# Kernel tuning notes

Hardware: AMD Instinct MI355X
Metric: run time of the kernel (lower is better)

## Reference

```python
import jax, jax.numpy as jnp
import numpy as np

EMBED = 768
HEADS = 12
HEAD_DIM = EMBED // HEADS
RATES = (1, 2, 4)
SEGS = (2048, 4096, 8192)


def setup_inputs() -> dict:
    key = jax.random.key(0)
    k1, k2, k3 = jax.random.split(key, 3)
    b, n = 2, 8192
    x = jax.random.normal(k1, (b, n, EMBED), dtype=jnp.float32)
    Wqkv = jax.random.normal(k2, (3 * EMBED, EMBED), dtype=jnp.float32) * 0.02
    Wout = jax.random.normal(k3, (EMBED, EMBED), dtype=jnp.float32) * 0.02
    return {"x": x, "Wqkv": Wqkv, "Wout": Wout}


def _dilated_attention(qkv):
    # qkv: [b, n, 3, h, d]
    b, n, _, h, d = qkv.shape
    scale = 1.0 / jnp.sqrt(jnp.asarray(d, qkv.dtype))
    out = jnp.zeros((b, n, h, d), dtype=qkv.dtype)
    for r, s in zip(RATES, SEGS):
        sr = s // r
        nseg = n // s
        # strided gather: [b, nseg, sr, 3, h, d]
        g = qkv.reshape(b, nseg, s, 3, h, d)[:, :, ::r]
        # fold stride offset into batch; attention runs over the segment axis
        g = g.transpose(0, 2, 1, 3, 4, 5).reshape(b * sr, nseg, 3, h, d)
        q, k, v = g[:, :, 0], g[:, :, 1], g[:, :, 2]
        scores = jnp.einsum('bnhd,bmhd->bhnm', q, k) * scale
        attn = jax.nn.softmax(scores, axis=-1)
        o = jnp.einsum('bhnm,bmhd->bnhd', attn, v)
        # scatter-add back into strided positions
        o = o.reshape(b, sr, nseg, h, d).transpose(0, 2, 1, 3, 4)
        out = out.reshape(b, nseg, s, h, d).at[:, :, ::r].add(o).reshape(b, n, h, d)
    # normalize over full sequence dim (as in original module)
    out = out / out.sum(axis=1, keepdims=True)
    return out


def reference(x, Wqkv, Wout):
    b, n, e = x.shape
    qkv = (x @ Wqkv.T).reshape(b, n, 3, HEADS, HEAD_DIM)
    o = _dilated_attention(qkv)  # [b, n, h, d]
    return o.reshape(b, n, e) @ Wout.T
```

## Files before the change

kernel.cpp:

```cpp
#include <hip/hip_runtime.h>

typedef unsigned short u16;
typedef __attribute__((ext_vector_type(8))) short bf16x8;
typedef __attribute__((ext_vector_type(4))) float f32x4;

__device__ __forceinline__ u16 f2bf_rne(float f) {
  unsigned u = __float_as_uint(f);
  u += 0x7fffu + ((u >> 16) & 1u);
  return (u16)(u >> 16);
}
__device__ __forceinline__ float bf2f(u16 h) {
  return __uint_as_float(((unsigned)h) << 16);
}
__device__ __forceinline__ void split1(float v, u16& h, u16& l) {
  u16 hh = f2bf_rne(v);
  h = hh;
  l = f2bf_rne(v - bf2f(hh));
}

__device__ __forceinline__ void gl16(const void* g, void* l) {
  __builtin_amdgcn_global_load_lds(
      (const __attribute__((address_space(1))) unsigned int*)g,
      (__attribute__((address_space(3))) unsigned int*)l,
      16, 0, 0);
}

__global__ void split_convert_all(const float4* __restrict__ x,
                                  ushort4* __restrict__ xhi, ushort4* __restrict__ xlo,
                                  const float4* __restrict__ wq,
                                  ushort4* __restrict__ wqh, ushort4* __restrict__ wql) {
  int i = blockIdx.x * 256 + threadIdx.x;
  const float4* src;
  ushort4 *dh, *dl;
  int idx;
  if (i < 3145728) { src = x; dh = xhi; dl = xlo; idx = i; }
  else if (i < 3588096) { src = wq; dh = wqh; dl = wql; idx = i - 3145728; }
  else return;
  float4 v = src[idx];
  ushort4 h, l;
  split1(v.x, h.x, l.x); split1(v.y, h.y, l.y);
  split1(v.z, h.z, l.z); split1(v.w, h.w, l.w);
  dh[idx] = h; dl[idx] = l;
}

__global__ __launch_bounds__(256, 2) void gemm_split_bt(
    const u16* __restrict__ Ahi, const u16* __restrict__ Alo, int lda,
    const u16* __restrict__ Bhi, const u16* __restrict__ Blo,
    const u16* __restrict__ Bhi2, const u16* __restrict__ Blo2,
    float* __restrict__ C, int M, int N, int K) {
  __shared__ __align__(16) u16 sAh[128 * 64], sAl[128 * 64], sBh[128 * 64], sBl[128 * 64];
  const int tid = threadIdx.x;
  const int wave = tid >> 6;
  const int lane = tid & 63;
  const int tm0 = blockIdx.x * 128;
  const int tn0 = blockIdx.y * 128;
  const int wm = (wave & 1) * 64;
  const int wn = (wave >> 1) * 64;
  if (2 * tm0 >= M) { Bhi = Bhi2; Blo = Blo2; }

  const int srow = wave * 32 + (lane >> 3);
  const int c = lane & 7;
  const int scol = (c ^ ((lane >> 3) & 7)) * 8;
  const u16* gAh = Ahi + (size_t)(tm0 + srow) * lda + scol;
  const u16* gAl = Alo + (size_t)(tm0 + srow) * lda + scol;
  const u16* gBh = Bhi + (size_t)(tn0 + srow) * K + scol;
  const u16* gBl = Blo + (size_t)(tn0 + srow) * K + scol;
  u16* lAh = &sAh[wave * 32 * 64];
  u16* lAl = &sAl[wave * 32 * 64];
  u16* lBh = &sBh[wave * 32 * 64];
  u16* lBl = &sBl[wave * 32 * 64];
  const size_t rstepA = (size_t)8 * lda;
  const size_t rstepB = (size_t)8 * K;

  f32x4 acc[4][4] = {};
  const int fr = lane & 15;
  const int quad = lane >> 4;

  for (int kt = 0; kt < K; kt += 64) {
#pragma unroll
    for (int r = 0; r < 4; ++r) {
      gl16(gAh + kt + r * rstepA, lAh + r * 512);
      gl16(gAl + kt + r * rstepA, lAl + r * 512);
      gl16(gBh + kt + r * rstepB, lBh + r * 512);
      gl16(gBl + kt + r * rstepB, lBl + r * 512);
    }
    __syncthreads();
    for (int subk = 0; subk < 2; ++subk) {
      const int k0 = ((subk * 4 + quad) ^ (fr & 7)) * 8;
      bf16x8 ah[4], al[4], bh[4], bl[4];
#pragma unroll
      for (int i = 0; i < 4; ++i) {
        ah[i] = *(const bf16x8*)&sAh[(wm + i * 16 + fr) * 64 + k0];
        al[i] = *(const bf16x8*)&sAl[(wm + i * 16 + fr) * 64 + k0];
        bh[i] = *(const bf16x8*)&sBh[(wn + i * 16 + fr) * 64 + k0];
        bl[i] = *(const bf16x8*)&sBl[(wn + i * 16 + fr) * 64 + k0];
      }
#pragma unroll
      for (int i = 0; i < 4; ++i)
#pragma unroll
        for (int j = 0; j < 4; ++j) {
          acc[i][j] = __builtin_amdgcn_mfma_f32_16x16x32_bf16(ah[i], bh[j], acc[i][j], 0, 0, 0);
          acc[i][j] = __builtin_amdgcn_mfma_f32_16x16x32_bf16(ah[i], bl[j], acc[i][j], 0, 0, 0);
          acc[i][j] = __builtin_amdgcn_mfma_f32_16x16x32_bf16(al[i], bh[j], acc[i][j], 0, 0, 0);
        }
    }
    __syncthreads();
  }

  const int col = lane & 15;
  const int rowq = (lane >> 4) * 4;
#pragma unroll
  for (int i = 0; i < 4; ++i)
#pragma unroll
    for (int j = 0; j < 4; ++j) {
      size_t base = (size_t)(tm0 + wm + i * 16 + rowq) * N + (tn0 + wn + j * 16 + col);
#pragma unroll
      for (int r = 0; r < 4; ++r) C[base + (size_t)r * N] = acc[i][j][r];
    }
}

__global__ __launch_bounds__(256) void attn_dilated(const float* __restrict__ qkv,
                                                    u16* __restrict__ qk16,
                                                    float* __restrict__ Spart) {
  __shared__ float rows[4][2312];
  __shared__ float sc[12][16];
  __shared__ float Aw[12][16];
  const int t = threadIdx.x;
  const int i0 = blockIdx.x;
  const int b = blockIdx.y;
  const size_t rowbase = (size_t)b * 8192 + i0;

  for (int idx = t; idx < 4 * 576; idx += 256) {
    int j = idx / 576, c4 = idx - j * 576;
    ((float4*)rows[j])[c4] = ((const float4*)(qkv + (rowbase + 2048 * j) * 2304))[c4];
  }
  __syncthreads();

  if (t < 192) {
    int h = t >> 4, j = (t >> 2) & 3, jp = t & 3;
    const float4* q = (const float4*)&rows[j][h * 64];
    const float4* k = (const float4*)&rows[jp][768 + h * 64];
    float s = 0.f;
#pragma unroll
    for (int d = 0; d < 16; ++d) {
      float4 a = q[d], bb = k[d];
      s += a.x * bb.x + a.y * bb.y + a.z * bb.z + a.w * bb.w;
    }
    sc[h][(j << 2) | jp] = s * 0.125f;
  }
  __syncthreads();

  if (t < 48) {
    int h = t >> 2, j = t & 3;
    float s0 = sc[h][j * 4 + 0], s1 = sc[h][j * 4 + 1];
    float s2 = sc[h][j * 4 + 2], s3 = sc[h][j * 4 + 3];
    float m = fmaxf(fmaxf(s0, s1), fmaxf(s2, s3));
    float e0 = expf(s0 - m), e1 = expf(s1 - m), e2 = expf(s2 - m), e3 = expf(s3 - m);
    float inv = 1.f / (e0 + e1 + e2 + e3);
    float a[4] = {e0 * inv, e1 * inv, e2 * inv, e3 * inv};
    if ((i0 & 1) == 0) {
      int p = j ^ 2;
      float ss = sc[h][j * 4 + j], sx = sc[h][j * 4 + p];
      float mm = fmaxf(ss, sx);
      float es = expf(ss - mm), ex = expf(sx - mm);
      float iv = 1.f / (es + ex);
      a[j] += es * iv;
      a[p] += ex * iv;
    }
    if ((i0 & 3) == 0) a[j] += 1.f;
    Aw[h][j * 4 + 0] = a[0]; Aw[h][j * 4 + 1] = a[1];
    Aw[h][j * 4 + 2] = a[2]; Aw[h][j * 4 + 3] = a[3];
  }
  __syncthreads();

  float* sp = Spart + ((size_t)b * 64 + (i0 & 63)) * 768;
#pragma unroll
  for (int rep = 0; rep < 3; ++rep) {
    int cc = rep * 256 + t;
    int h = cc >> 6;
    float ps = 0.f;
#pragma unroll
    for (int j = 0; j < 4; ++j) {
      float v = 0.f;
#pragma unroll
      for (int jp = 0; jp < 4; ++jp) v = fmaf(Aw[h][(j << 2) | jp], rows[jp][1536 + cc], v);
      u16 h16, l16;
      split1(v, h16, l16);
      size_t base = (rowbase + 2048 * j) * 4608;
      qk16[base + cc] = h16;
      qk16[base + 768 + cc] = l16;
      ps += v;
    }
    atomicAdd(&sp[cc], ps);
  }
}

__global__ void colred(const float* __restrict__ Spart, float* __restrict__ Sinv) {
  int i = blockIdx.x * 256 + threadIdx.x;
  if (i >= 1536) return;
  int b = i / 768, c = i - b * 768;
  const float* p = Spart + (size_t)b * 64 * 768 + c;
  float s = 0.f;
#pragma unroll
  for (int g = 0; g < 64; ++g) s += p[g * 768];
  Sinv[i] = 1.0f / s;
}

__global__ void scale_wout(const float4* __restrict__ Wout, const float* __restrict__ Sinv,
                           ushort4* __restrict__ wh0, ushort4* __restrict__ wl0,
                           ushort4* __restrict__ wh1, ushort4* __restrict__ wl1) {
  int i = blockIdx.x * 256 + threadIdx.x;
  if (i >= 294912) return;
  int b = i / 147456;
  int r = i - b * 147456;
  int c = (r % 192) * 4;
  const float* s = Sinv + b * 768 + c;
  float4 v = Wout[r];
  v.x *= s[0]; v.y *= s[1]; v.z *= s[2]; v.w *= s[3];
  ushort4 h, l;
  split1(v.x, h.x, l.x); split1(v.y, h.y, l.y);
  split1(v.z, h.z, l.z); split1(v.w, h.w, l.w);
  if (b == 0) { wh0[r] = h; wl0[r] = l; }
  else        { wh1[r] = h; wl1[r] = l; }
}

extern "C" void kernel_launch(void* const* d_in, const int* in_sizes, int n_in,
                              void* d_out, int out_size, void* d_ws, size_t ws_size,
                              hipStream_t stream) {
  (void)in_sizes; (void)n_in; (void)out_size; (void)ws_size;
  const float* x = (const float*)d_in[0];
  const float* Wqkv = (const float*)d_in[1];
  const float* Wout = (const float*)d_in[2];
  float* out = (float*)d_out;

  char* w = (char*)d_ws;
  float* qkv = (float*)(w);
  u16* qk16 = (u16*)(w);
  size_t off = 150994944;
  u16* xhi = (u16*)(w + off);
  float* Spart = (float*)(w + off);
  float* Sinv = (float*)(w + off + 393216);
  u16* wh0 = (u16*)(w + off + 400000);
  u16* wl0 = (u16*)(w + off + 1579648);
  u16* wh1 = (u16*)(w + off + 2759296);
  u16* wl1 = (u16*)(w + off + 3938944);
  off += 25165824;
  u16* xlo = (u16*)(w + off); off += 25165824;
  u16* wqh = (u16*)(w + off); off += 3538944;
  u16* wql = (u16*)(w + off); off += 3538944;

  split_convert_all<<<dim3(14016), 256, 0, stream>>>(
      (const float4*)x, (ushort4*)xhi, (ushort4*)xlo,
      (const float4*)Wqkv, (ushort4*)wqh, (ushort4*)wql);

  gemm_split_bt<<<dim3(128, 18), 256, 0, stream>>>(xhi, xlo, 768, wqh, wql, wqh, wql,
                                                   qkv, 16384, 2304, 768);

  hipMemsetAsync(Spart, 0, 393216, stream);
  attn_dilated<<<dim3(2048, 2), 256, 0, stream>>>(qkv, qk16, Spart);

  colred<<<dim3(6), 256, 0, stream>>>(Spart, Sinv);

  scale_wout<<<dim3(1152), 256, 0, stream>>>((const float4*)Wout, Sinv,
                                             (ushort4*)wh0, (ushort4*)wl0,
                                             (ushort4*)wh1, (ushort4*)wl1);

  gemm_split_bt<<<dim3(128, 6), 256, 0, stream>>>(qk16, qk16 + 768, 4608,
                                                  wh0, wl0, wh1, wl1,
                                                  out, 16384, 768, 768);
}
```

Baseline: 351.4 us.

## Make split-bf16 GEMM persistent with double-buffered LDS prefetch

Converts the split-precision GEMM into a persistent kernel with a fixed grid of 512 blocks that walks output tiles in a strided loop. The K step drops from 64 to 32, and LDS is double-buffered so the global-to-LDS loads for the next K slice, or the first slice of the next tile, are issued while the current slice is computed. This hides load latency and cuts the barriers per iteration to one, at the cost of more loop iterations, a new swizzle pattern and possibly lower occupancy or tail imbalance.

```diff
diff --git a/kernel.cpp b/kernel.cpp
--- a/kernel.cpp
+++ b/kernel.cpp
@@ -47,53 +47,62 @@
     const u16* __restrict__ Ahi, const u16* __restrict__ Alo, int lda,
     const u16* __restrict__ Bhi, const u16* __restrict__ Blo,
     const u16* __restrict__ Bhi2, const u16* __restrict__ Blo2,
-    float* __restrict__ C, int M, int N, int K) {
-  __shared__ __align__(16) u16 sAh[128 * 64], sAl[128 * 64], sBh[128 * 64], sBl[128 * 64];
+    float* __restrict__ C, int M, int N, int K, int ntiles) {
+  __shared__ __align__(16) u16 lds[2][4][128 * 32];
   const int tid = threadIdx.x;
   const int wave = tid >> 6;
   const int lane = tid & 63;
-  const int tm0 = blockIdx.x * 128;
-  const int tn0 = blockIdx.y * 128;
   const int wm = (wave & 1) * 64;
   const int wn = (wave >> 1) * 64;
-  if (2 * tm0 >= M) { Bhi = Bhi2; Blo = Blo2; }
-
-  const int srow = wave * 32 + (lane >> 3);
-  const int c = lane & 7;
-  const int scol = (c ^ ((lane >> 3) & 7)) * 8;
-  const u16* gAh = Ahi + (size_t)(tm0 + srow) * lda + scol;
-  const u16* gAl = Alo + (size_t)(tm0 + srow) * lda + scol;
-  const u16* gBh = Bhi + (size_t)(tn0 + srow) * K + scol;
-  const u16* gBl = Blo + (size_t)(tn0 + srow) * K + scol;
-  u16* lAh = &sAh[wave * 32 * 64];
-  u16* lAl = &sAl[wave * 32 * 64];
-  u16* lBh = &sBh[wave * 32 * 64];
-  u16* lBl = &sBl[wave * 32 * 64];
-  const size_t rstepA = (size_t)8 * lda;
-  const size_t rstepB = (size_t)8 * K;
-
-  f32x4 acc[4][4] = {};
+  const int swrow = wave * 32 + (lane >> 2);
+  const int sscol = ((lane & 3) ^ ((lane >> 3) & 3)) * 8;
+  const int woff = wave * 1024;
+
+  auto stage = [&](int buf, int tt, int kt) {
+    const int bx = tt & 127, by = tt >> 7;
+    const u16* pbh = (2 * (bx * 128) >= M) ? Bhi2 : Bhi;
+    const u16* pbl = (2 * (bx * 128) >= M) ? Blo2 : Blo;
+    const size_t aoff = (size_t)(bx * 128 + swrow) * lda + sscol + kt;
+    const size_t boff = (size_t)(by * 128 + swrow) * K + sscol + kt;
+    u16* d0 = &lds[buf][0][woff];
+    u16* d1 = &lds[buf][1][woff];
+    u16* d2 = &lds[buf][2][woff];
+    u16* d3 = &lds[buf][3][woff];
+    gl16(Ahi + aoff, d0);
+    gl16(Ahi + aoff + (size_t)16 * lda, d0 + 512);
+    gl16(Alo + aoff, d1);
+    gl16(Alo + aoff + (size_t)16 * lda, d1 + 512);
+    gl16(pbh + boff, d2);
+    gl16(pbh + boff + (size_t)16 * K, d2 + 512);
+    gl16(pbl + boff, d3);
+    gl16(pbl + boff + (size_t)16 * K, d3 + 512);
+  };
+
   const int fr = lane & 15;
   const int quad = lane >> 4;
-
-  for (int kt = 0; kt < K; kt += 64) {
-#pragma unroll
-    for (int r = 0; r < 4; ++r) {
-      gl16(gAh + kt + r * rstepA, lAh + r * 512);
-      gl16(gAl + kt + r * rstepA, lAl + r * 512);
-      gl16(gBh + kt + r * rstepB, lBh + r * 512);
-      gl16(gBl + kt + r * rstepB, lBl + r * 512);
-    }
-    __syncthreads();
-    for (int subk = 0; subk < 2; ++subk) {
-      const int k0 = ((subk * 4 + quad) ^ (fr & 7)) * 8;
+  const int k0 = (quad ^ ((fr >> 1) & 3)) * 8;
+  const int gstride = gridDim.x;
+
+  int t = blockIdx.x;
+  if (t >= ntiles) return;
+  stage(0, t, 0);
+  int cur = 0;
+  for (; t < ntiles; t += gstride) {
+    const int tm0 = (t & 127) * 128;
+    const int tn0 = (t >> 7) * 128;
+    f32x4 acc[4][4] = {};
+    for (int kt = 0; kt < K; kt += 32) {
+      __syncthreads();
+      if (kt + 32 < K) stage(cur ^ 1, t, kt + 32);
+      else if (t + gstride < ntiles) stage(cur ^ 1, t + gstride, 0);
+      const u16* base = &lds[cur][0][0];
       bf16x8 ah[4], al[4], bh[4], bl[4];
 #pragma unroll
       for (int i = 0; i < 4; ++i) {
-        ah[i] = *(const bf16x8*)&sAh[(wm + i * 16 + fr) * 64 + k0];
-        al[i] = *(const bf16x8*)&sAl[(wm + i * 16 + fr) * 64 + k0];
-        bh[i] = *(const bf16x8*)&sBh[(wn + i * 16 + fr) * 64 + k0];
-        bl[i] = *(const bf16x8*)&sBl[(wn + i * 16 + fr) * 64 + k0];
+        ah[i] = *(const bf16x8*)&base[0 * 4096 + (wm + i * 16 + fr) * 32 + k0];
+        al[i] = *(const bf16x8*)&base[1 * 4096 + (wm + i * 16 + fr) * 32 + k0];
+        bh[i] = *(const bf16x8*)&base[2 * 4096 + (wn + i * 16 + fr) * 32 + k0];
+        bl[i] = *(const bf16x8*)&base[3 * 4096 + (wn + i * 16 + fr) * 32 + k0];
       }
 #pragma unroll
       for (int i = 0; i < 4; ++i)
@@ -103,20 +112,19 @@
           acc[i][j] = __builtin_amdgcn_mfma_f32_16x16x32_bf16(ah[i], bl[j], acc[i][j], 0, 0, 0);
           acc[i][j] = __builtin_amdgcn_mfma_f32_16x16x32_bf16(al[i], bh[j], acc[i][j], 0, 0, 0);
         }
-    }
-    __syncthreads();
-  }
-
-  const int col = lane & 15;
-  const int rowq = (lane >> 4) * 4;
-#pragma unroll
-  for (int i = 0; i < 4; ++i)
-#pragma unroll
-    for (int j = 0; j < 4; ++j) {
-      size_t base = (size_t)(tm0 + wm + i * 16 + rowq) * N + (tn0 + wn + j * 16 + col);
-#pragma unroll
-      for (int r = 0; r < 4; ++r) C[base + (size_t)r * N] = acc[i][j][r];
-    }
+      cur ^= 1;
+    }
+    const int col = lane & 15;
+    const int rowq = quad * 4;
+#pragma unroll
+    for (int i = 0; i < 4; ++i)
+#pragma unroll
+      for (int j = 0; j < 4; ++j) {
+        size_t basec = (size_t)(tm0 + wm + i * 16 + rowq) * N + (tn0 + wn + j * 16 + col);
+#pragma unroll
+        for (int r = 0; r < 4; ++r) C[basec + (size_t)r * N] = acc[i][j][r];
+      }
+  }
 }
 
 __global__ __launch_bounds__(256) void attn_dilated(const float* __restrict__ qkv,
@@ -253,8 +261,8 @@
       (const float4*)x, (ushort4*)xhi, (ushort4*)xlo,
       (const float4*)Wqkv, (ushort4*)wqh, (ushort4*)wql);
 
-  gemm_split_bt<<<dim3(128, 18), 256, 0, stream>>>(xhi, xlo, 768, wqh, wql, wqh, wql,
-                                                   qkv, 16384, 2304, 768);
+  gemm_split_bt<<<dim3(512), 256, 0, stream>>>(xhi, xlo, 768, wqh, wql, wqh, wql,
+                                               qkv, 16384, 2304, 768, 2304);
 
   hipMemsetAsync(Spart, 0, 393216, stream);
   attn_dilated<<<dim3(2048, 2), 256, 0, stream>>>(qkv, qk16, Spart);
@@ -265,7 +273,7 @@
                                              (ushort4*)wh0, (ushort4*)wl0,
                                              (ushort4*)wh1, (ushort4*)wl1);
 
-  gemm_split_bt<<<dim3(128, 6), 256, 0, stream>>>(qk16, qk16 + 768, 4608,
-                                                  wh0, wl0, wh1, wl1,
-                                                  out, 16384, 768, 768);
-}
+  gemm_split_bt<<<dim3(512), 256, 0, stream>>>(qk16, qk16 + 768, 4608,
+                                               wh0, wl0, wh1, wl1,
+                                               out, 16384, 768, 768, 768);
+}
```

New measurement: 372.5 us. 6.0% more time.
